# Kernel optimization log

Measured on AMD Instinct MI355X. Metric: run time of the kernel, lower is better.

The kernel has to match this reference:

```python
import jax, jax.numpy as jnp
import numpy as np

B, H, S, D = 2, 16, 2048, 64  # batch, heads, seq (n_qry == n_tok), head_dim


def setup_inputs() -> dict:
    key = jax.random.key(0)
    kq, kk, kv = jax.random.split(key, 3)
    Q = jax.random.normal(kq, (B, H, S, D), dtype=jnp.float32)
    K_cache = jax.random.normal(kk, (B, H, S, D), dtype=jnp.float32)
    V_cache = jax.random.normal(kv, (B, H, S, D), dtype=jnp.float32)
    return {"Q": Q, "K_cache": K_cache, "V_cache": V_cache}


def reference(Q, K_cache, V_cache):
    n_qry = Q.shape[-2]
    n_tok = K_cache.shape[-2]
    scale = 1.0 / jnp.sqrt(jnp.asarray(Q.shape[-1], Q.dtype))
    # [B, H, n_qry, n_tok] scores
    A = jnp.einsum('bhqd,bhkd->bhqk', Q, K_cache) * scale
    # causal mask: query q may attend key k iff k <= q + (n_tok - n_qry)
    q_idx = jnp.arange(n_qry)[:, None]
    k_idx = jnp.arange(n_tok)[None, :]
    mask = k_idx <= q_idx + (n_tok - n_qry)
    A = jnp.where(mask, A, -jnp.inf)
    P = jax.nn.softmax(A, axis=-1)
    return jnp.einsum('bhqk,bhkd->bhqd', P, V_cache)
```

## Files before the change

### kernel.cpp

```cpp
#include <hip/hip_runtime.h>

typedef __attribute__((ext_vector_type(8))) short bf16x8;
typedef __attribute__((ext_vector_type(4))) float f32x4;

#define NB 2
#define NH 16
#define NS 2048
#define ND 64
#define NBH 32
#define QSCALE (0.125f * 1.44269504088896f)
#define CMAX 12.0f

static __device__ __forceinline__ unsigned pack2(float lo, float hi) {
  return __builtin_amdgcn_perm(__builtin_bit_cast(unsigned, hi),
                               __builtin_bit_cast(unsigned, lo), 0x07060302u);
}


__global__ __launch_bounds__(256) void prep_kernel(const float* __restrict__ K,
                                                   const float* __restrict__ V,
                                                   short* __restrict__ W) {
  const int xcd = blockIdx.x & 7;
  const int rest = blockIdx.x >> 3;
  const int lb = rest >> 5;
  const int kb = rest & 31;
  const int bh = xcd * 4 + lb;
  const float* Kp = K + (size_t)bh * NS * ND + (size_t)kb * 64 * ND;
  const float* Vp = V + (size_t)bh * NS * ND + (size_t)kb * 64 * ND;
  short* Wp = W + ((size_t)bh * 32 + kb) * 8192;

  __shared__ float vt[64 * 65];

  {
    int vrow = threadIdx.x >> 2, seg = threadIdx.x & 3;
    const float* src = Vp + vrow * ND + seg * 16;
    float* dst = vt + vrow * 65 + seg * 16;
#pragma unroll
    for (int i = 0; i < 4; ++i) {
      float4 v = *(const float4*)(src + i * 4);
      dst[i * 4 + 0] = v.x; dst[i * 4 + 1] = v.y;
      dst[i * 4 + 2] = v.z; dst[i * 4 + 3] = v.w;
    }
  }

#pragma unroll
  for (int e0 = 0; e0 < 512; e0 += 256) {
    int e = e0 + threadIdx.x;
    int c = e >> 6, lane = e & 63;
    int st = c >> 1, cc = c & 1, quad = lane >> 4, col = lane & 15;
    int prow = 32 * (st >> 1) + 8 * (col >> 2) + 4 * (st & 1) + (col & 3);
    const float* kr = Kp + prow * ND + cc * 32 + quad * 8;
    float4 a = *(const float4*)kr;
    float4 b = *(const float4*)(kr + 4);
    uint4 u = {pack2(a.x, a.y), pack2(a.z, a.w), pack2(b.x, b.y), pack2(b.z, b.w)};
    *(uint4*)(Wp + (size_t)e * 8) = u;
  }
  __syncthreads();

#pragma unroll
  for (int e0 = 0; e0 < 512; e0 += 256) {
    int e = e0 + threadIdx.x;
    int c = e >> 6, lane = e & 63;
    int g = c >> 2, t = c & 3, quad = lane >> 4, col = lane & 15;
    const float* base = vt + (32 * g + 8 * quad) * 65 + t * 16 + col;
    float f[8];
#pragma unroll
    for (int j = 0; j < 8; ++j) f[j] = base[j * 65];
    uint4 u = {pack2(f[0], f[1]), pack2(f[2], f[3]),
               pack2(f[4], f[5]), pack2(f[6], f[7])};
    *(uint4*)(Wp + 4096 + (size_t)e * 8) = u;
  }
}

__global__ __launch_bounds__(256, 2) void fa_kernel(
    const float* __restrict__ Q, const short* __restrict__ W,
    float* __restrict__ O) {
  const int lane = threadIdx.x & 63;
  const int wave = threadIdx.x >> 6;
  const int col  = lane & 15;
  const int quad = lane >> 4;

  const int i = blockIdx.x;
  const int phase = i >> 8;
  const int rr_ = i & 255;
  const int xcd = rr_ & 7;
  const int s5 = rr_ >> 3;
  const int bh = xcd * 4 + (s5 & 3);
  const int pp = s5 >> 2;
  const int pr = phase ? (15 - pp) : pp;
  const int stepsA = pr + 1;
  const int TOT = 32 - pr;
  const int myTile  = (wave < 2) ? pr : (31 - pr);
  const int mySteps = (wave < 2) ? stepsA : TOT;
  const int qhalf = wave & 1;

  __shared__ short Kbuf[4][4096];
  __shared__ short Vbuf[4][4096];

  const float* Qp = Q + (size_t)bh * NS * ND;
  const short* Wb = W + (size_t)bh * 32 * 8192;
  float*       Op = O + (size_t)bh * NS * ND;

  bf16x8 qf[2][2];
#pragma unroll
  for (int f = 0; f < 2; ++f) {
    const float* qrow =
        Qp + (size_t)(myTile * 64 + qhalf * 32 + f * 16 + col) * ND + quad * 8;
#pragma unroll
    for (int c = 0; c < 2; ++c) {
      float4 a = *(const float4*)(qrow + c * 32);
      float4 b = *(const float4*)(qrow + c * 32 + 4);
      union { bf16x8 v; unsigned u[4]; } t;
      t.u[0] = pack2(a.x * QSCALE, a.y * QSCALE);
      t.u[1] = pack2(a.z * QSCALE, a.w * QSCALE);
      t.u[2] = pack2(b.x * QSCALE, b.y * QSCALE);
      t.u[3] = pack2(b.z * QSCALE, b.w * QSCALE);
      qf[f][c] = t.v;
    }
  }

  f32x4 o4[2][4];
#pragma unroll
  for (int f = 0; f < 2; ++f)
#pragma unroll
    for (int t = 0; t < 4; ++t) o4[f][t] = (f32x4){0.f, 0.f, 0.f, 0.f};
  float lsum[2] = {0.f, 0.f};

  auto stage = [&](int s, int b) {
    const short* base = Wb + (size_t)s * 8192;
#pragma unroll
    for (int ii = 0; ii < 4; ++ii) {
      int id = wave * 4 + ii;
      const short* g = base + id * 512 + lane * 8;
      __attribute__((address_space(3))) void* dst =
          (id < 8)
              ? (__attribute__((address_space(3))) void*)&Kbuf[b][id * 512]
              : (__attribute__((address_space(3))) void*)&Vbuf[b][(id - 8) * 512];
      __builtin_amdgcn_global_load_lds(
          (const __attribute__((address_space(1))) void*)g, dst, 16, 0, 0);
    }
  };

  stage(0, 0);
  stage(1, 1);
  stage(2, 2);

  for (int s = 0; s < TOT; ++s) {
    asm volatile("s_waitcnt vmcnt(8)" ::: "memory");
    asm volatile("s_barrier" ::: "memory");
    if (s + 3 < TOT) stage(s + 3, (s + 3) & 3);
    const int b = s & 3;

    if (s < mySteps) {
      const bool last = (s == mySteps - 1);

      float sc[2][4][4];
#pragma unroll
      for (int st = 0; st < 4; ++st) {
        bf16x8 k0 = *(const bf16x8*)&Kbuf[b][(st * 2 + 0) * 512 + lane * 8];
        bf16x8 k1 = *(const bf16x8*)&Kbuf[b][(st * 2 + 1) * 512 + lane * 8];
#pragma unroll
        for (int f = 0; f < 2; ++f) {
          f32x4 acc = (f32x4){-CMAX, -CMAX, -CMAX, -CMAX};
          acc = __builtin_amdgcn_mfma_f32_16x16x32_bf16(k0, qf[f][0], acc, 0, 0, 0);
          acc = __builtin_amdgcn_mfma_f32_16x16x32_bf16(k1, qf[f][1], acc, 0, 0, 0);
#pragma unroll
          for (int r = 0; r < 4; ++r) sc[f][st][r] = acc[r];
        }
      }

      if (last) {
#pragma unroll
        for (int f = 0; f < 2; ++f) {
          int qin = qhalf * 32 + f * 16 + col;
#pragma unroll
          for (int st = 0; st < 4; ++st)
#pragma unroll
            for (int r = 0; r < 4; ++r) {
              int phys = 32 * (st >> 1) + 8 * quad + 4 * (st & 1) + r;
              if (phys > qin) sc[f][st][r] = -INFINITY;
            }
        }
      }

      bf16x8 pf[2][2];
#pragma unroll
      for (int f = 0; f < 2; ++f)
#pragma unroll
        for (int g = 0; g < 2; ++g) {
          float p0 = __builtin_amdgcn_exp2f(sc[f][2 * g + 0][0]);
          float p1 = __builtin_amdgcn_exp2f(sc[f][2 * g + 0][1]);
          float p2 = __builtin_amdgcn_exp2f(sc[f][2 * g + 0][2]);
          float p3 = __builtin_amdgcn_exp2f(sc[f][2 * g + 0][3]);
          float p4 = __builtin_amdgcn_exp2f(sc[f][2 * g + 1][0]);
          float p5 = __builtin_amdgcn_exp2f(sc[f][2 * g + 1][1]);
          float p6 = __builtin_amdgcn_exp2f(sc[f][2 * g + 1][2]);
          float p7 = __builtin_amdgcn_exp2f(sc[f][2 * g + 1][3]);
          lsum[f] += ((p0 + p1) + (p2 + p3)) + ((p4 + p5) + (p6 + p7));
          union { bf16x8 v; unsigned u[4]; } t;
          t.u[0] = pack2(p0, p1);
          t.u[1] = pack2(p2, p3);
          t.u[2] = pack2(p4, p5);
          t.u[3] = pack2(p6, p7);
          pf[f][g] = t.v;
        }

#pragma unroll
      for (int g = 0; g < 2; ++g)
#pragma unroll
        for (int t = 0; t < 4; ++t) {
          bf16x8 vf = *(const bf16x8*)&Vbuf[b][(g * 4 + t) * 512 + lane * 8];
#pragma unroll
          for (int f = 0; f < 2; ++f)
            o4[f][t] = __builtin_amdgcn_mfma_f32_16x16x32_bf16(pf[f][g], vf,
                                                               o4[f][t], 0, 0, 0);
        }

      if (last) {
#pragma unroll
        for (int f = 0; f < 2; ++f) {
          float lt = lsum[f];
          lt += __shfl_xor(lt, 16, 64);
          lt += __shfl_xor(lt, 32, 64);
#pragma unroll
          for (int r = 0; r < 4; ++r) {
            float lr = __shfl(lt, quad * 4 + r, 64);
            float inv = 1.0f / lr;
            float* orow = Op + (size_t)(myTile * 64 + qhalf * 32 + f * 16 +
                                        quad * 4 + r) * ND + col;
#pragma unroll
            for (int t = 0; t < 4; ++t) orow[t * 16] = o4[f][t][r] * inv;
          }
        }
      }
    }
  }
}

extern "C" void kernel_launch(void* const* d_in, const int* in_sizes, int n_in,
                              void* d_out, int out_size, void* d_ws, size_t ws_size,
                              hipStream_t stream) {
  const float* Q = (const float*)d_in[0];
  const float* K = (const float*)d_in[1];
  const float* V = (const float*)d_in[2];
  short* W = (short*)d_ws;
  hipLaunchKernelGGL(prep_kernel, dim3(NBH * 32), dim3(256), 0, stream, K, V, W);
  hipLaunchKernelGGL(fa_kernel, dim3(512), dim3(256), 0, stream, Q, W,
                     (float*)d_out);
}
```

Measured before the change: 122.9 us.

## Load K/V tiles directly into registers per wave, dropping shared-memory staging

Removes the LDS ring buffer, global_load_lds staging and per-step block barriers. Each wave now owns a 32-row query group and streams K and V fragments straight from global memory into registers, double-buffering K for the next tile. The work mapping also changes from paired short/long tiles per block to four consecutive query groups per block. This drops synchronisation and LDS traffic, but every wave now fetches K/V separately, which multiplies L2 traffic and register pressure, and waves within a block have unequal trip counts.

```diff
diff --git a/kernel.cpp b/kernel.cpp
--- a/kernel.cpp
+++ b/kernel.cpp
@@ -81,21 +81,15 @@
   const int quad = lane >> 4;
 
   const int i = blockIdx.x;
-  const int phase = i >> 8;
-  const int rr_ = i & 255;
-  const int xcd = rr_ & 7;
-  const int s5 = rr_ >> 3;
-  const int bh = xcd * 4 + (s5 & 3);
-  const int pp = s5 >> 2;
-  const int pr = phase ? (15 - pp) : pp;
-  const int stepsA = pr + 1;
-  const int TOT = 32 - pr;
-  const int myTile  = (wave < 2) ? pr : (31 - pr);
-  const int mySteps = (wave < 2) ? stepsA : TOT;
-  const int qhalf = wave & 1;
-
-  __shared__ short Kbuf[4][4096];
-  __shared__ short Vbuf[4][4096];
+  const int xcd = i & 7;
+  const int j = i >> 3;
+  const int phase = j >> 5;
+  const int slot = j & 31;
+  const int bh = xcd * 4 + (slot & 3);
+  const int rblk = slot >> 2;
+  const int r = phase ? (15 - rblk) : rblk;
+  const int qg = r * 4 + wave;
+  const int T = (qg >> 1) + 1;
 
   const float* Qp = Q + (size_t)bh * NS * ND;
   const short* Wb = W + (size_t)bh * 32 * 8192;
@@ -104,8 +98,7 @@
   bf16x8 qf[2][2];
 #pragma unroll
   for (int f = 0; f < 2; ++f) {
-    const float* qrow =
-        Qp + (size_t)(myTile * 64 + qhalf * 32 + f * 16 + col) * ND + quad * 8;
+    const float* qrow = Qp + (size_t)(qg * 32 + f * 16 + col) * ND + quad * 8;
 #pragma unroll
     for (int c = 0; c < 2; ++c) {
       float4 a = *(const float4*)(qrow + c * 32);
@@ -126,113 +119,105 @@
     for (int t = 0; t < 4; ++t) o4[f][t] = (f32x4){0.f, 0.f, 0.f, 0.f};
   float lsum[2] = {0.f, 0.f};
 
-  auto stage = [&](int s, int b) {
-    const short* base = Wb + (size_t)s * 8192;
-#pragma unroll
-    for (int ii = 0; ii < 4; ++ii) {
-      int id = wave * 4 + ii;
-      const short* g = base + id * 512 + lane * 8;
-      __attribute__((address_space(3))) void* dst =
-          (id < 8)
-              ? (__attribute__((address_space(3))) void*)&Kbuf[b][id * 512]
-              : (__attribute__((address_space(3))) void*)&Vbuf[b][(id - 8) * 512];
-      __builtin_amdgcn_global_load_lds(
-          (const __attribute__((address_space(1))) void*)g, dst, 16, 0, 0);
-    }
-  };
-
-  stage(0, 0);
-  stage(1, 1);
-  stage(2, 2);
-
-  for (int s = 0; s < TOT; ++s) {
-    asm volatile("s_waitcnt vmcnt(8)" ::: "memory");
-    asm volatile("s_barrier" ::: "memory");
-    if (s + 3 < TOT) stage(s + 3, (s + 3) & 3);
-    const int b = s & 3;
-
-    if (s < mySteps) {
-      const bool last = (s == mySteps - 1);
-
-      float sc[2][4][4];
-#pragma unroll
-      for (int st = 0; st < 4; ++st) {
-        bf16x8 k0 = *(const bf16x8*)&Kbuf[b][(st * 2 + 0) * 512 + lane * 8];
-        bf16x8 k1 = *(const bf16x8*)&Kbuf[b][(st * 2 + 1) * 512 + lane * 8];
-#pragma unroll
-        for (int f = 0; f < 2; ++f) {
-          f32x4 acc = (f32x4){-CMAX, -CMAX, -CMAX, -CMAX};
-          acc = __builtin_amdgcn_mfma_f32_16x16x32_bf16(k0, qf[f][0], acc, 0, 0, 0);
-          acc = __builtin_amdgcn_mfma_f32_16x16x32_bf16(k1, qf[f][1], acc, 0, 0, 0);
-#pragma unroll
-          for (int r = 0; r < 4; ++r) sc[f][st][r] = acc[r];
-        }
-      }
-
-      if (last) {
-#pragma unroll
-        for (int f = 0; f < 2; ++f) {
-          int qin = qhalf * 32 + f * 16 + col;
-#pragma unroll
-          for (int st = 0; st < 4; ++st)
-#pragma unroll
-            for (int r = 0; r < 4; ++r) {
-              int phys = 32 * (st >> 1) + 8 * quad + 4 * (st & 1) + r;
-              if (phys > qin) sc[f][st][r] = -INFINITY;
-            }
-        }
-      }
-
-      bf16x8 pf[2][2];
-#pragma unroll
-      for (int f = 0; f < 2; ++f)
-#pragma unroll
-        for (int g = 0; g < 2; ++g) {
-          float p0 = __builtin_amdgcn_exp2f(sc[f][2 * g + 0][0]);
-          float p1 = __builtin_amdgcn_exp2f(sc[f][2 * g + 0][1]);
-          float p2 = __builtin_amdgcn_exp2f(sc[f][2 * g + 0][2]);
-          float p3 = __builtin_amdgcn_exp2f(sc[f][2 * g + 0][3]);
-          float p4 = __builtin_amdgcn_exp2f(sc[f][2 * g + 1][0]);
-          float p5 = __builtin_amdgcn_exp2f(sc[f][2 * g + 1][1]);
-          float p6 = __builtin_amdgcn_exp2f(sc[f][2 * g + 1][2]);
-          float p7 = __builtin_amdgcn_exp2f(sc[f][2 * g + 1][3]);
-          lsum[f] += ((p0 + p1) + (p2 + p3)) + ((p4 + p5) + (p6 + p7));
-          union { bf16x8 v; unsigned u[4]; } t;
-          t.u[0] = pack2(p0, p1);
-          t.u[1] = pack2(p2, p3);
-          t.u[2] = pack2(p4, p5);
-          t.u[3] = pack2(p6, p7);
-          pf[f][g] = t.v;
-        }
-
-#pragma unroll
-      for (int g = 0; g < 2; ++g)
-#pragma unroll
-        for (int t = 0; t < 4; ++t) {
-          bf16x8 vf = *(const bf16x8*)&Vbuf[b][(g * 4 + t) * 512 + lane * 8];
-#pragma unroll
-          for (int f = 0; f < 2; ++f)
-            o4[f][t] = __builtin_amdgcn_mfma_f32_16x16x32_bf16(pf[f][g], vf,
-                                                               o4[f][t], 0, 0, 0);
-        }
-
-      if (last) {
-#pragma unroll
-        for (int f = 0; f < 2; ++f) {
-          float lt = lsum[f];
-          lt += __shfl_xor(lt, 16, 64);
-          lt += __shfl_xor(lt, 32, 64);
-#pragma unroll
-          for (int r = 0; r < 4; ++r) {
-            float lr = __shfl(lt, quad * 4 + r, 64);
-            float inv = 1.0f / lr;
-            float* orow = Op + (size_t)(myTile * 64 + qhalf * 32 + f * 16 +
-                                        quad * 4 + r) * ND + col;
-#pragma unroll
-            for (int t = 0; t < 4; ++t) orow[t * 16] = o4[f][t][r] * inv;
+  bf16x8 kr[2][8];
+#pragma unroll
+  for (int c = 0; c < 8; ++c)
+    kr[0][c] = *(const bf16x8*)(Wb + c * 512 + lane * 8);
+
+  for (int t = 0; t < T; ++t) {
+    const int cur = t & 1, nxt = cur ^ 1;
+    const short* base = Wb + (size_t)t * 8192;
+
+    bf16x8 vr[8];
+#pragma unroll
+    for (int c = 0; c < 8; ++c)
+      vr[c] = *(const bf16x8*)(base + 4096 + c * 512 + lane * 8);
+
+    if (t + 1 < T) {
+      const short* kb = Wb + (size_t)(t + 1) * 8192;
+#pragma unroll
+      for (int c = 0; c < 8; ++c)
+        kr[nxt][c] = *(const bf16x8*)(kb + c * 512 + lane * 8);
+    }
+
+    const bool last = (t == T - 1);
+
+    float sc[2][4][4];
+#pragma unroll
+    for (int st = 0; st < 4; ++st) {
+      bf16x8 k0 = kr[cur][st * 2 + 0];
+      bf16x8 k1 = kr[cur][st * 2 + 1];
+#pragma unroll
+      for (int f = 0; f < 2; ++f) {
+        f32x4 acc = (f32x4){-CMAX, -CMAX, -CMAX, -CMAX};
+        acc = __builtin_amdgcn_mfma_f32_16x16x32_bf16(k0, qf[f][0], acc, 0, 0, 0);
+        acc = __builtin_amdgcn_mfma_f32_16x16x32_bf16(k1, qf[f][1], acc, 0, 0, 0);
+#pragma unroll
+        for (int rr = 0; rr < 4; ++rr) sc[f][st][rr] = acc[rr];
+      }
+    }
+
+    if (last) {
+#pragma unroll
+      for (int f = 0; f < 2; ++f) {
+        int qrel = (qg & 1) * 32 + f * 16 + col;
+#pragma unroll
+        for (int st = 0; st < 4; ++st)
+#pragma unroll
+          for (int rr = 0; rr < 4; ++rr) {
+            int phys = 32 * (st >> 1) + 8 * quad + 4 * (st & 1) + rr;
+            if (phys > qrel) sc[f][st][rr] = -INFINITY;
           }
-        }
-      }
+      }
+    }
+
+    bf16x8 pf[2][2];
+#pragma unroll
+    for (int f = 0; f < 2; ++f)
+#pragma unroll
+      for (int g = 0; g < 2; ++g) {
+        float p0 = __builtin_amdgcn_exp2f(sc[f][2 * g + 0][0]);
+        float p1 = __builtin_amdgcn_exp2f(sc[f][2 * g + 0][1]);
+        float p2 = __builtin_amdgcn_exp2f(sc[f][2 * g + 0][2]);
+        float p3 = __builtin_amdgcn_exp2f(sc[f][2 * g + 0][3]);
+        float p4 = __builtin_amdgcn_exp2f(sc[f][2 * g + 1][0]);
+        float p5 = __builtin_amdgcn_exp2f(sc[f][2 * g + 1][1]);
+        float p6 = __builtin_amdgcn_exp2f(sc[f][2 * g + 1][2]);
+        float p7 = __builtin_amdgcn_exp2f(sc[f][2 * g + 1][3]);
+        lsum[f] += ((p0 + p1) + (p2 + p3)) + ((p4 + p5) + (p6 + p7));
+        union { bf16x8 v; unsigned u[4]; } tt;
+        tt.u[0] = pack2(p0, p1);
+        tt.u[1] = pack2(p2, p3);
+        tt.u[2] = pack2(p4, p5);
+        tt.u[3] = pack2(p6, p7);
+        pf[f][g] = tt.v;
+      }
+
+#pragma unroll
+    for (int g = 0; g < 2; ++g)
+#pragma unroll
+      for (int t4 = 0; t4 < 4; ++t4) {
+        bf16x8 vf = vr[g * 4 + t4];
+#pragma unroll
+        for (int f = 0; f < 2; ++f)
+          o4[f][t4] = __builtin_amdgcn_mfma_f32_16x16x32_bf16(pf[f][g], vf,
+                                                              o4[f][t4], 0, 0, 0);
+      }
+  }
+
+#pragma unroll
+  for (int f = 0; f < 2; ++f) {
+    float lt = lsum[f];
+    lt += __shfl_xor(lt, 16, 64);
+    lt += __shfl_xor(lt, 32, 64);
+#pragma unroll
+    for (int rr = 0; rr < 4; ++rr) {
+      float lr = __shfl(lt, quad * 4 + rr, 64);
+      float inv = 1.0f / lr;
+      float* orow =
+          Op + (size_t)(qg * 32 + f * 16 + quad * 4 + rr) * ND + col;
+#pragma unroll
+      for (int t4 = 0; t4 < 4; ++t4) orow[t4 * 16] = o4[f][t4][rr] * inv;
     }
   }
 }
```

After: 185.8 us. +51.2%, slower.
